# Performance work log

Measured on AMD Instinct MI355X. Metric: run time of the kernel, lower is better.

Reference implementation:

```python
import jax, jax.numpy as jnp
import numpy as np
from jax import lax

N, T, E = 20000, 64, 640000
H, OUT, HEADS = 128, 64, 3
NEG_SLOPE = 0.2  # GATConv default negative_slope


def setup_inputs() -> dict:
    key = jax.random.key(0)
    ks = jax.random.split(key, 10)
    s = 0.1
    return {
        "node_features": jax.random.normal(ks[0], (N, T), jnp.float32),
        "edge_index": jax.random.randint(ks[1], (2, E), 0, N, dtype=jnp.int32),
        "edge_attributes": jax.random.uniform(ks[2], (E,), jnp.float32),
        "lstm_Wih": jax.random.normal(ks[3], (4 * H, 1), jnp.float32) * s,
        "lstm_Whh": jax.random.normal(ks[4], (4 * H, H), jnp.float32) * s,
        "lstm_bih": jnp.zeros((4 * H,), jnp.float32),
        "lstm_bhh": jnp.zeros((4 * H,), jnp.float32),
        "gcn_W": jax.random.normal(ks[5], (H, H), jnp.float32) * s,
        "gcn_b": jnp.zeros((H,), jnp.float32),
        "gat_W": jax.random.normal(ks[6], (HEADS * OUT, H), jnp.float32) * s,
        "gat_att_src": jax.random.normal(ks[7], (HEADS, OUT), jnp.float32) * s,
        "gat_att_dst": jax.random.normal(ks[8], (HEADS, OUT), jnp.float32) * s,
        "gat_b": jnp.zeros((HEADS * OUT,), jnp.float32),
    }


def _lstm_last(x, Wih, Whh, bih, bhh):
    """x: [N, T, 1] -> last hidden state [N, H] (torch gate order i,f,g,o)."""
    n = x.shape[0]
    h_dim = Whh.shape[1]
    b = bih + bhh

    def step(carry, xt):
        h, c = carry
        g = xt @ Wih.T + h @ Whh.T + b  # [N, 4H]
        i, f, gg, o = jnp.split(g, 4, axis=-1)
        c = jax.nn.sigmoid(f) * c + jax.nn.sigmoid(i) * jnp.tanh(gg)
        h = jax.nn.sigmoid(o) * jnp.tanh(c)
        return (h, c), None

    init = (jnp.zeros((n, h_dim), x.dtype), jnp.zeros((n, h_dim), x.dtype))
    (h, _), _ = lax.scan(step, init, jnp.swapaxes(x, 0, 1))
    return h


def _add_self_loops(row, col, n):
    loop = jnp.arange(n, dtype=row.dtype)
    return jnp.concatenate([row, loop]), jnp.concatenate([col, loop])


def _gcn(x, row, col, edge_weight, W, b):
    """PyG GCNConv: self-loops (weight 1), symmetric normalization, W x + b."""
    n = x.shape[0]
    row, col = _add_self_loops(row, col, n)
    ew = jnp.concatenate([edge_weight, jnp.ones((n,), edge_weight.dtype)])
    x = x @ W.T  # [N, H]
    deg = jax.ops.segment_sum(ew, col, num_segments=n)
    dinv = jnp.where(deg > 0, deg ** -0.5, 0.0)
    norm = dinv[row] * ew * dinv[col]  # [E+N]
    out = jax.ops.segment_sum(x[row] * norm[:, None], col, num_segments=n)
    return out + b


def _gat(x, row, col, W, att_src, att_dst, b):
    """PyG GATConv (concat=True): self-loops, edge softmax over incoming edges."""
    n = x.shape[0]
    heads, c = att_src.shape
    xh = (x @ W.T).reshape(n, heads, c)  # [N, Hd, C]
    a_src = jnp.einsum('nhc,hc->nh', xh, att_src)  # [N, Hd]
    a_dst = jnp.einsum('nhc,hc->nh', xh, att_dst)
    row, col = _add_self_loops(row, col, n)
    alpha = jax.nn.leaky_relu(a_src[row] + a_dst[col], NEG_SLOPE)  # [E', Hd]
    amax = jax.ops.segment_max(alpha, col, num_segments=n)
    alpha = jnp.exp(alpha - amax[col])
    denom = jax.ops.segment_sum(alpha, col, num_segments=n)
    alpha = alpha / denom[col]
    out = jax.ops.segment_sum(xh[row] * alpha[:, :, None], col, num_segments=n)
    return out.reshape(n, heads * c) + b


def reference(node_features, edge_index, edge_attributes,
              lstm_Wih, lstm_Whh, lstm_bih, lstm_bhh,
              gcn_W, gcn_b, gat_W, gat_att_src, gat_att_dst, gat_b):
    x = node_features[:, :, None]  # [N, T, 1]
    x = _lstm_last(x, lstm_Wih, lstm_Whh, lstm_bih, lstm_bhh)  # [N, H]
    x = jax.nn.relu(x)
    row, col = edge_index[0], edge_index[1]
    x = _gcn(x, row, col, edge_attributes, gcn_W, gcn_b)
    x = jax.nn.relu(x)
    x = _gat(x, row, col, gat_W, gat_att_src, gat_att_dst, gat_b)  # [N, Hd*C]
    return jnp.mean(x, axis=0, keepdims=True)  # global_mean_pool, batch=None -> [1, Hd*C]
```

## Files before the change

### kernel.cpp

```cpp
#include <hip/hip_runtime.h>


#define N_NODES 20000
#define T_STEPS 64
#define N_EDGES 640000
#define HDIM    128
#define JOUT    192
#define NEG_SLOPE 0.2f
#define EDGE_CAP 128
#define NBW     16
#define NGRP    5
#define NBB     (NBW * NGRP)
#define BTHR    640
#define NBLK    250
#define GRIDX   256
#define LDS_W     131072
#define LDS_BW    4096
#define LDS_SCR   (NGRP * 4096)
#define LDS_FLG   256
#define LDS_TOTAL (LDS_W + LDS_BW + LDS_SCR + LDS_FLG)

#define L2E  1.4426950408889634f
#define K2E  2.8853900817779268f

typedef _Float16 half8 __attribute__((ext_vector_type(8)));
typedef _Float16 half4v __attribute__((ext_vector_type(4)));
typedef _Float16 half2v __attribute__((ext_vector_type(2)));
typedef float floatx4 __attribute__((ext_vector_type(4)));

__device__ __forceinline__ float lrelu(float x) { return x > 0.f ? x : NEG_SLOPE * x; }

__global__ __launch_bounds__(256) void prep_kernel(
    const float* __restrict__ Whh, _Float16* __restrict__ Wpack,
    const float* __restrict__ gcnW, _Float16* __restrict__ WpackG,
    const float* __restrict__ gatW, _Float16* __restrict__ WpackA,
    int* __restrict__ cnt, float* __restrict__ Wgt, float* __restrict__ accum)
{
  const int b = blockIdx.x;
  const int tid = threadIdx.x;
  if (b < 32) {
    int i = b * 256 + tid;
    int tile = i >> 6, lane = i & 63;
    int nt = tile >> 2, kt = tile & 3;
    int row = nt * 16 + (lane & 15);
    int c0  = kt * 32 + (lane >> 4) * 8;
    const float sc = ((row >> 7) == 2) ? K2E : L2E;
    half8 v;
    #pragma unroll
    for (int j = 0; j < 8; ++j)
      v[j] = (_Float16)(Whh[row * 128 + c0 + j] * sc);
    *(half8*)&Wpack[(size_t)i * 8] = v;
  } else if (b < 40) {
    int i = (b - 32) * 256 + tid;
    int tile = i >> 6, lane = i & 63;
    int mt = tile >> 2, kt = tile & 3;
    int row = mt * 16 + (lane & 15);
    int c0  = kt * 32 + (lane >> 4) * 8;
    half8 v;
    #pragma unroll
    for (int j = 0; j < 8; ++j) v[j] = (_Float16)gcnW[row * 128 + c0 + j];
    *(half8*)&WpackG[(size_t)i * 8] = v;
  } else if (b < 52) {
    int i = (b - 40) * 256 + tid;
    int tile = i >> 6, lane = i & 63;
    int mt = tile >> 2, kt = tile & 3;
    int row = mt * 16 + (lane & 15);
    int c0  = kt * 32 + (lane >> 4) * 8;
    half8 v;
    #pragma unroll
    for (int j = 0; j < 8; ++j) v[j] = (_Float16)gatW[row * 128 + c0 + j];
    *(half8*)&WpackA[(size_t)i * 8] = v;
  } else {
    int i = (b - 52) * 256 + tid;
    if (i < N_NODES) {
      cnt[i] = 0;
      *(float4*)&Wgt[i * 4] = make_float4(0.f, 0.f, 0.f, 0.f);
    }
    if (i < JOUT) accum[i] = 0.f;
  }
}


#define INITACC(L, acc) do {                                                  \
  _Pragma("unroll") for (int g_ = 0; g_ < 4; ++g_) {                          \
    const float4 p0_ = *(const float4*)&bwRole[g_ * 128 + (L) * 16];          \
    const float4 p1_ = *(const float4*)&bwRole[g_ * 128 + (L) * 16 + 2];      \
    acc[g_][0] = p0_.x + xv * p0_.y;                                          \
    acc[g_][1] = p0_.z + xv * p0_.w;                                          \
    acc[g_][2] = p1_.x + xv * p1_.y;                                          \
    acc[g_][3] = p1_.z + xv * p1_.w;                                          \
  }                                                                           \
} while (0)

#define LDA(buf, L, KT) do {                                                  \
  _Pragma("unroll") for (int g_ = 0; g_ < 4; ++g_)                            \
    buf[g_] = *(const half8*)&WlRole[g_ * 16384 + (L) * 2048 + (KT) * 512];   \
} while (0)

#define MFA(acc, buf, KT) do {                                                \
  _Pragma("unroll") for (int g_ = 0; g_ < 4; ++g_)                            \
    acc[g_] = __builtin_amdgcn_mfma_f32_16x16x32_f16(                         \
        buf[g_], Bf[(KT)], acc[g_], 0, 0, 0);                                 \
} while (0)

#define PHASE4(L, acc) do {                                                   \
  const int cg_ = cgb + (L);                                                  \
  half4v hpack;                                                               \
  _Pragma("unroll") for (int r_ = 0; r_ < 4; ++r_) {                          \
    const float Be = __builtin_amdgcn_exp2f(-acc[0][r_]);                     \
    const float Ae = __builtin_amdgcn_exp2f(-acc[1][r_]);                     \
    const float De = __builtin_amdgcn_exp2f(acc[2][r_]);                      \
    const float Ee = __builtin_amdgcn_exp2f(-acc[3][r_]);                     \
    const float Ap = Ae + 1.f;                                                \
    const float Bp = Be + 1.f;                                                \
    const float Dp = De + 1.f;                                                \
    const float Nn = cst[(L) * 4 + r_] * Bp * Dp + Ap * (De - 1.f);           \
    const float cv = Nn * __builtin_amdgcn_rcpf(Ap * Bp * Dp);                \
    cst[(L) * 4 + r_] = cv;                                                   \
    const float cvc = fminf(fmaxf(cv, -10.f), 10.f);                          \
    const float Fe = __builtin_amdgcn_exp2f(K2E * cvc);                       \
    hpack[r_] = (_Float16)((Fe - 1.f) *                                       \
                __builtin_amdgcn_rcpf((Ee + 1.f) * (Fe + 1.f)));              \
  }                                                                           \
  const int lp_ = nl + 16 * (2 * (cg_ & 1) + wq_hi);                          \
  *(half4v*)&myscr[(cg_ >> 1) * 512 + lp_ * 8 + j0] = hpack;                  \
} while (0)

#define SB __builtin_amdgcn_sched_barrier(0)

#define SIGNAL(arr, val) do {                                                 \
  __threadfence_block();                                                      \
  if (ln == 0) arr[wv] = (val);                                               \
} while (0)
#define WAITGE(arr, val) do {                                                 \
  if (ln == 0) { while (arr[pw] < (val)) __builtin_amdgcn_s_sleep(1); }       \
  __builtin_amdgcn_wave_barrier();                                            \
  __threadfence_block();                                                      \
} while (0)

#define LSTM_STEP(t) do {                                                     \
  WAITGE(flW, (t));                                                           \
  half8 Bf[4];                                                                \
  _Pragma("unroll") for (int kt_ = 0; kt_ < 4; ++kt_)                         \
    Bf[kt_] = *(const half8*)&scrLane[kt_ * 512];                             \
  SIGNAL(flR, (t) + 1);                                                       \
  floatx4 accA[4], accB[4];                                                   \
  half8 Aa[4], Ab[4];                                                         \
                                                                  \
  INITACC(0, accA);                                                           \
  LDA(Aa, 0, 0); LDA(Ab, 0, 1);                                               \
  MFA(accA, Aa, 0); LDA(Aa, 0, 2);                                            \
  MFA(accA, Ab, 1); LDA(Ab, 0, 3);                                            \
  MFA(accA, Aa, 2); MFA(accA, Ab, 3);                                         \
                                                                  \
  INITACC(1, accB); LDA(Aa, 1, 0); LDA(Ab, 1, 1);                             \
  WAITGE(flR, (t) + 1);                                                       \
  SB; PHASE4(0, accA);                                                        \
  MFA(accB, Aa, 0); LDA(Aa, 1, 2);                                            \
  MFA(accB, Ab, 1); LDA(Ab, 1, 3);                                            \
  MFA(accB, Aa, 2); MFA(accB, Ab, 3);                                         \
                                                                  \
  INITACC(2, accA); LDA(Aa, 2, 0); LDA(Ab, 2, 1);                             \
  SB; PHASE4(1, accB);                                                        \
  MFA(accA, Aa, 0); LDA(Aa, 2, 2);                                            \
  MFA(accA, Ab, 1); LDA(Ab, 2, 3);                                            \
  MFA(accA, Aa, 2); MFA(accA, Ab, 3);                                         \
                                                                  \
  INITACC(3, accB); LDA(Aa, 3, 0); LDA(Ab, 3, 1);                             \
  SB; PHASE4(2, accA);                                                        \
  MFA(accB, Aa, 0); LDA(Aa, 3, 2);                                            \
  MFA(accB, Ab, 1); LDA(Ab, 3, 3);                                            \
  MFA(accB, Aa, 2); MFA(accB, Ab, 3);                                         \
  PHASE4(3, accB);                                                            \
  SIGNAL(flW, (t) + 1);                                                       \
} while (0)

__global__ __attribute__((amdgpu_flat_work_group_size(BTHR, BTHR),
                          amdgpu_waves_per_eu(3, 3)))
void lstm_stream_kernel(
    const float* __restrict__ xfeat, const _Float16* __restrict__ Wpack,
    const float* __restrict__ Wih, const float* __restrict__ bih,
    const float* __restrict__ bhh, _Float16* __restrict__ x1,
    const int* __restrict__ ei, const float* __restrict__ ew,
    int* __restrict__ cnt, int2* __restrict__ pairB)
{
  const int tid  = threadIdx.x;

  if (blockIdx.x >= NBLK) {
    const int stride = (GRIDX - NBLK) * BTHR;
    for (int e = (blockIdx.x - NBLK) * BTHR + tid; e < N_EDGES; e += stride) {
      const int r = ei[e];
      const int c = ei[N_EDGES + e];
      const float w = ew[e];
      const int p = atomicAdd(&cnt[c], 1);
      pairB[(size_t)c * EDGE_CAP + p] = make_int2(r, __float_as_int(w));
    }
    return;
  }

  extern __shared__ char dynlds[];
  _Float16* Wl  = (_Float16*)dynlds;
  float2*   bw  = (float2*)(dynlds + LDS_W);
  _Float16* scr = (_Float16*)(dynlds + LDS_W + LDS_BW);
  volatile int* flR = (volatile int*)(dynlds + LDS_W + LDS_BW + LDS_SCR);
  volatile int* flW = flR + 16;

  const int wv   = tid >> 6;
  const int pw   = wv ^ 1;
  const int grp  = wv >> 1;
  const int role = wv & 1;
  const int cgb  = role * 4;
  const int ln   = tid & 63;
  const int nl   = ln & 15;
  const int quad = ln >> 4;
  const int n0   = blockIdx.x * NBB + grp * NBW;

  {
    const float4* src = (const float4*)Wpack;
    float4* dst = (float4*)Wl;
    for (int i = tid; i < LDS_W / 16; i += BTHR) dst[i] = src[i];
  }
  for (int i = tid; i < 512; i += BTHR) {
    const float sc = ((i >> 7) == 2) ? K2E : L2E;
    bw[i] = make_float2((bih[i] + bhh[i]) * sc, Wih[i] * sc);
  }
  {
    float4* z = (float4*)scr;
    for (int i = tid; i < LDS_SCR / 16; i += BTHR)
      z[i] = make_float4(0.f, 0.f, 0.f, 0.f);
  }
  if (tid < 32) { flR[tid] = 0; flW[tid] = 0; }
  __syncthreads();

  _Float16* myscr = scr + grp * 2048;
  const _Float16* WlRole  = Wl + (size_t)cgb * 2048 + (size_t)ln * 8;
  const float2*   bwRole  = bw + cgb * 16 + quad * 4;
  const _Float16* scrLane = myscr + (size_t)ln * 8;
  const float* xrow = xfeat + (size_t)(n0 + nl) * T_STEPS;

  float cst[16];
  #pragma unroll
  for (int i = 0; i < 16; ++i) cst[i] = 0.f;

  const int wq_hi = quad >> 1;
  const int j0    = (quad & 1) * 4;

  float xv = xrow[0];

  #pragma unroll 1
  for (int t = 0; t < T_STEPS; ++t) {
    const float xn = xrow[(t + 1 <= 63) ? (t + 1) : 63];
    LSTM_STEP(t);
    xv = xn;
  }

  #pragma unroll
  for (int k = 0; k < 2; ++k) {
    const int kt = role * 2 + k;
    half8 hf = *(const half8*)&scrLane[kt * 512];
    #pragma unroll
    for (int j = 0; j < 8; ++j)
      hf[j] = (_Float16)fmaxf((float)hf[j], 0.f);
    *(half8*)&x1[(size_t)(n0 + nl) * HDIM + kt * 32 + quad * 8] = hf;
  }
}

__global__ __launch_bounds__(256) void degdinv_kernel(
    const int* __restrict__ cnt, const int2* __restrict__ pairB,
    float* __restrict__ dinv)
{
  const int lane = threadIdx.x & 63;
  const int wv = threadIdx.x >> 6;
  const int c = blockIdx.x * 4 + wv;
  const int cc = cnt[c];
  const size_t base = (size_t)c * EDGE_CAP;
  float s = 0.f;
  for (int k = lane; k < cc; k += 64)
    s += __int_as_float(pairB[base + k].y);
  #pragma unroll
  for (int off = 1; off < 64; off <<= 1) s += __shfl_xor(s, off);
  if (lane == 0) dinv[c] = rsqrtf(s + 1.0f);
}

__global__ __launch_bounds__(256) void agg_gemm_att_kernel(
    const _Float16* __restrict__ x1, const float* __restrict__ dinv,
    const int* __restrict__ cnt, const int2* __restrict__ pairB,
    const float* __restrict__ gcn_b,
    const _Float16* __restrict__ PG, const _Float16* __restrict__ PA,
    const float* __restrict__ att_src, const float* __restrict__ att_dst,
    _Float16* __restrict__ xh, float4* __restrict__ asrc,
    float4* __restrict__ adst)
{
  __shared__ float2 stg[4][64];
  __shared__ _Float16 z[16][132];
  __shared__ _Float16 zz[16][132];
  __shared__ float aS[JOUT], aD[JOUT];
  __shared__ float sAp[4][16][3], sDp[4][16][3];

  const int tid = threadIdx.x;
  const int ln = tid & 63;
  const int wv = tid >> 6;
  const int quad = ln >> 4;
  const int nl = ln & 15;
  const int nb = blockIdx.x * 16;

  for (int i = tid; i < JOUT; i += 256) { aS[i] = att_src[i]; aD[i] = att_dst[i]; }

  const half2v* x12 = (const half2v*)x1;
  #pragma unroll 1
  for (int d = 0; d < 4; ++d) {
    const int c = nb + wv * 4 + d;
    const float dc = dinv[c];
    const half2v xc = x12[c * 64 + ln];
    float ax = (float)xc[0] * dc * dc, ay = (float)xc[1] * dc * dc;
    const int cc = cnt[c];
    const size_t base = (size_t)c * EDGE_CAP;
    for (int tb = 0; tb < cc; tb += 64) {
      const int ne = min(64, cc - tb);
      const int k = tb + ln;
      if (k < cc) {
        const int2 pr = pairB[base + k];
        stg[wv][ln] = make_float2(__int_as_float(pr.x),
                                  __int_as_float(pr.y) * dinv[pr.x] * dc);
      }
      __builtin_amdgcn_wave_barrier();
      int i = 0;
      for (; i + 4 <= ne; i += 4) {
        float2 p0 = stg[wv][i],     p1 = stg[wv][i + 1];
        float2 p2 = stg[wv][i + 2], p3 = stg[wv][i + 3];
        const half2v a0 = x12[(size_t)__float_as_int(p0.x) * 64 + ln];
        const half2v a1 = x12[(size_t)__float_as_int(p1.x) * 64 + ln];
        const half2v a2 = x12[(size_t)__float_as_int(p2.x) * 64 + ln];
        const half2v a3 = x12[(size_t)__float_as_int(p3.x) * 64 + ln];
        ax += (float)a0[0] * p0.y + (float)a1[0] * p1.y +
              (float)a2[0] * p2.y + (float)a3[0] * p3.y;
        ay += (float)a0[1] * p0.y + (float)a1[1] * p1.y +
              (float)a2[1] * p2.y + (float)a3[1] * p3.y;
      }
      for (; i < ne; ++i) {
        float2 p0 = stg[wv][i];
        const half2v a0 = x12[(size_t)__float_as_int(p0.x) * 64 + ln];
        ax += (float)a0[0] * p0.y; ay += (float)a0[1] * p0.y;
      }
      __builtin_amdgcn_wave_barrier();
    }
    const int dn = wv * 4 + d;
    half2v o; o[0] = (_Float16)ax; o[1] = (_Float16)ay;
    *(half2v*)&z[dn][ln * 2] = o;
  }
  __syncthreads();

  {
    half8 Bf[4];
    #pragma unroll
    for (int kt = 0; kt < 4; ++kt)
      Bf[kt] = *(const half8*)&z[nl][kt * 32 + quad * 8];
    #pragma unroll
    for (int mm = 0; mm < 2; ++mm) {
      const int m = wv * 2 + mm;
      floatx4 acc = {0.f, 0.f, 0.f, 0.f};
      #pragma unroll
      for (int kt = 0; kt < 4; ++kt) {
        const half8 Af = *(const half8*)&PG[(size_t)((m * 4 + kt) * 64 + ln) * 8];
        acc = __builtin_amdgcn_mfma_f32_16x16x32_f16(Af, Bf[kt], acc, 0, 0, 0);
      }
      #pragma unroll
      for (int j = 0; j < 4; ++j) {
        const int jj = m * 16 + quad * 4 + j;
        zz[nl][jj] = (_Float16)fmaxf(acc[j] + gcn_b[jj], 0.f);
      }
    }
  }
  __syncthreads();

  {
    half8 Bf[4];
    #pragma unroll
    for (int kt = 0; kt < 4; ++kt)
      Bf[kt] = *(const half8*)&zz[nl][kt * 32 + quad * 8];
    float sA[3] = {0.f, 0.f, 0.f}, sD[3] = {0.f, 0.f, 0.f};
    #pragma unroll
    for (int mm = 0; mm < 3; ++mm) {
      const int m = wv * 3 + mm;
      floatx4 acc = {0.f, 0.f, 0.f, 0.f};
      #pragma unroll
      for (int kt = 0; kt < 4; ++kt) {
        const half8 Af = *(const half8*)&PA[(size_t)((m * 4 + kt) * 64 + ln) * 8];
        acc = __builtin_amdgcn_mfma_f32_16x16x32_f16(Af, Bf[kt], acc, 0, 0, 0);
      }
      const int h  = m >> 2;
      const int jo = (m & 3) * 16 + quad * 4;
      half4v o;
      #pragma unroll
      for (int j = 0; j < 4; ++j) {
        sA[h] += acc[j] * aS[h * 64 + jo + j];
        sD[h] += acc[j] * aD[h * 64 + jo + j];
        o[j] = (_Float16)acc[j];
      }
      *(half4v*)&xh[(size_t)(nb + nl) * JOUT + m * 16 + quad * 4] = o;
    }
    #pragma unroll
    for (int h = 0; h < 3; ++h) {
      sA[h] += __shfl_xor(sA[h], 16); sA[h] += __shfl_xor(sA[h], 32);
      sD[h] += __shfl_xor(sD[h], 16); sD[h] += __shfl_xor(sD[h], 32);
    }
    if (quad == 0) {
      #pragma unroll
      for (int h = 0; h < 3; ++h) {
        sAp[wv][nl][h] = sA[h];
        sDp[wv][nl][h] = sD[h];
      }
    }
  }
  __syncthreads();
  if (tid < 16) {
    float a0 = 0.f, a1 = 0.f, a2 = 0.f, d0 = 0.f, d1 = 0.f, d2 = 0.f;
    #pragma unroll
    for (int w = 0; w < 4; ++w) {
      a0 += sAp[w][tid][0]; a1 += sAp[w][tid][1]; a2 += sAp[w][tid][2];
      d0 += sDp[w][tid][0]; d1 += sDp[w][tid][1]; d2 += sDp[w][tid][2];
    }
    asrc[nb + tid] = make_float4(a0, a1, a2, 0.f);
    adst[nb + tid] = make_float4(d0, d1, d2, 0.f);
  }
}

__global__ __launch_bounds__(256) void gat_weight_kernel(
    const float4* __restrict__ asrc, const float4* __restrict__ adst,
    const int* __restrict__ cnt, const int2* __restrict__ pairB,
    float* __restrict__ W)
{
  const int lane = threadIdx.x & 63;
  const int wv = threadIdx.x >> 6;
  const int c = blockIdx.x * 4 + wv;
  const int cc = cnt[c];
  const size_t base = (size_t)c * EDGE_CAP;
  const float4 adc = adst[c];
  const float4 asc = asrc[c];
  const float se0 = __expf(lrelu(asc.x + adc.x));
  const float se1 = __expf(lrelu(asc.y + adc.y));
  const float se2 = __expf(lrelu(asc.z + adc.z));
  float dp0 = 0.f, dp1 = 0.f, dp2 = 0.f;
  float a0v[2], a1v[2], a2v[2]; int sv[2];
  #pragma unroll
  for (int it = 0; it < 2; ++it) {
    const int k = it * 64 + lane;
    sv[it] = -1;
    a0v[it] = 0.f; a1v[it] = 0.f; a2v[it] = 0.f;
    if (k < cc) {
      const int s = pairB[base + k].x;
      const float4 av = asrc[s];
      const float a0 = __expf(lrelu(av.x + adc.x));
      const float a1 = __expf(lrelu(av.y + adc.y));
      const float a2 = __expf(lrelu(av.z + adc.z));
      dp0 += a0; dp1 += a1; dp2 += a2;
      sv[it] = s; a0v[it] = a0; a1v[it] = a1; a2v[it] = a2;
    }
  }
  #pragma unroll
  for (int off = 1; off < 64; off <<= 1) {
    dp0 += __shfl_xor(dp0, off);
    dp1 += __shfl_xor(dp1, off);
    dp2 += __shfl_xor(dp2, off);
  }
  const float iv0 = 1.f / (dp0 + se0);
  const float iv1 = 1.f / (dp1 + se1);
  const float iv2 = 1.f / (dp2 + se2);
  if (lane == 0) {
    atomicAdd(&W[c * 4 + 0], se0 * iv0);
    atomicAdd(&W[c * 4 + 1], se1 * iv1);
    atomicAdd(&W[c * 4 + 2], se2 * iv2);
  }
  #pragma unroll
  for (int it = 0; it < 2; ++it) {
    if (sv[it] >= 0) {
      atomicAdd(&W[sv[it] * 4 + 0], a0v[it] * iv0);
      atomicAdd(&W[sv[it] * 4 + 1], a1v[it] * iv1);
      atomicAdd(&W[sv[it] * 4 + 2], a2v[it] * iv2);
    }
  }
}

__global__ __launch_bounds__(192) void gat_final_kernel(
    const _Float16* __restrict__ xh, const float* __restrict__ W,
    float* __restrict__ accum)
{
  const int j = threadIdx.x;
  const int h = j >> 6;
  float sum = 0.f;
  const int s0 = blockIdx.x * 80;
  for (int s = s0; s < s0 + 80; ++s)
    sum += W[s * 4 + h] * (float)xh[(size_t)s * JOUT + j];
  atomicAdd(&accum[j], sum);
}

__global__ void finalize_kernel(const float* __restrict__ accum,
                                const float* __restrict__ gat_b,
                                float* __restrict__ out)
{
  int j = threadIdx.x;
  if (j < JOUT) out[j] = accum[j] * (1.0f / N_NODES) + gat_b[j];
}

extern "C" void kernel_launch(void* const* d_in, const int* in_sizes, int n_in,
                              void* d_out, int out_size, void* d_ws, size_t ws_size,
                              hipStream_t stream)
{
  const float* xfeat = (const float*)d_in[0];
  const int*   eidx  = (const int*)d_in[1];
  const float* eattr = (const float*)d_in[2];
  const float* Wih   = (const float*)d_in[3];
  const float* Whh   = (const float*)d_in[4];
  const float* bihp  = (const float*)d_in[5];
  const float* bhhp  = (const float*)d_in[6];
  const float* gcnW  = (const float*)d_in[7];
  const float* gcnb  = (const float*)d_in[8];
  const float* gatW  = (const float*)d_in[9];
  const float* attS  = (const float*)d_in[10];
  const float* attD  = (const float*)d_in[11];
  const float* gatb  = (const float*)d_in[12];
  float* out = (float*)d_out;

  char* ws = (char*)d_ws;
  size_t off = 0;
  auto alloc = [&](size_t bytes) {
    char* p = ws + off;
    off += (bytes + 255) & ~size_t(255);
    return p;
  };
  _Float16*  x1     = (_Float16*)alloc((size_t)N_NODES * 128 * 2);
  _Float16*  xh     = (_Float16*)alloc((size_t)N_NODES * 192 * 2);
  float4*    asrc   = (float4*)alloc((size_t)N_NODES * 16);
  float4*    adst   = (float4*)alloc((size_t)N_NODES * 16);
  float*     dinv   = (float*)alloc((size_t)N_NODES * 4);
  int*       cnt    = (int*)alloc((size_t)N_NODES * 4);
  int2*      pairB  = (int2*)alloc((size_t)N_NODES * EDGE_CAP * 8);
  float*     Wgt    = (float*)alloc((size_t)N_NODES * 4 * 4);
  float*     accum  = (float*)alloc(JOUT * 4);
  _Float16*  wpack  = (_Float16*)alloc(131072);
  _Float16*  wpackG = (_Float16*)alloc((size_t)128 * 128 * 2);
  _Float16*  wpackA = (_Float16*)alloc((size_t)192 * 128 * 2);

  hipFuncSetAttribute((const void*)lstm_stream_kernel,
                      hipFuncAttributeMaxDynamicSharedMemorySize, LDS_TOTAL);

  prep_kernel<<<131, 256, 0, stream>>>(Whh, wpack, gcnW, wpackG, gatW, wpackA,
                                       cnt, Wgt, accum);
  lstm_stream_kernel<<<GRIDX, BTHR, LDS_TOTAL, stream>>>(
      xfeat, wpack, Wih, bihp, bhhp, x1, eidx, eattr, cnt, pairB);
  degdinv_kernel<<<N_NODES / 4, 256, 0, stream>>>(cnt, pairB, dinv);
  agg_gemm_att_kernel<<<N_NODES / 16, 256, 0, stream>>>(
      x1, dinv, cnt, pairB, gcnb, wpackG, wpackA, attS, attD, xh, asrc, adst);
  gat_weight_kernel<<<N_NODES / 4, 256, 0, stream>>>(asrc, adst, cnt, pairB, Wgt);
  gat_final_kernel<<<N_NODES / 80, 192, 0, stream>>>(xh, Wgt, accum);
  finalize_kernel<<<1, 256, 0, stream>>>(accum, gatb, out);
}
```

Baseline: 554.9 us.

## Split LSTM handshake into half-ready flags and fold degree into edge bucketing

```diff
diff --git a/kernel.cpp b/kernel.cpp
--- a/kernel.cpp
+++ b/kernel.cpp
@@ -34,7 +34,8 @@
     const float* __restrict__ Whh, _Float16* __restrict__ Wpack,
     const float* __restrict__ gcnW, _Float16* __restrict__ WpackG,
     const float* __restrict__ gatW, _Float16* __restrict__ WpackA,
-    int* __restrict__ cnt, float* __restrict__ Wgt, float* __restrict__ accum)
+    int* __restrict__ cnt, float* __restrict__ deg,
+    float* __restrict__ Wgt, float* __restrict__ accum)
 {
   const int b = blockIdx.x;
   const int tid = threadIdx.x;
@@ -74,6 +75,7 @@
     int i = (b - 52) * 256 + tid;
     if (i < N_NODES) {
       cnt[i] = 0;
+      deg[i] = 0.f;
       *(float4*)&Wgt[i * 4] = make_float4(0.f, 0.f, 0.f, 0.f);
     }
     if (i < JOUT) accum[i] = 0.f;
@@ -138,20 +140,24 @@
   __threadfence_block();                                                      \
 } while (0)
 
-#define LSTM_STEP(t) do {                                                     \
-  WAITGE(flW, (t));                                                           \
+#define LSTM_STEP(t, K0, K1, K2, K3) do {                                     \
   half8 Bf[4];                                                                \
-  _Pragma("unroll") for (int kt_ = 0; kt_ < 4; ++kt_)                         \
-    Bf[kt_] = *(const half8*)&scrLane[kt_ * 512];                             \
-  SIGNAL(flR, (t) + 1);                                                       \
+  Bf[K0] = *(const half8*)&scrLane[(K0) * 512];                               \
+  Bf[K1] = *(const half8*)&scrLane[(K1) * 512];                               \
   floatx4 accA[4], accB[4];                                                   \
   half8 Aa[4], Ab[4];                                                         \
-                                                                  \
+              \
   INITACC(0, accA);                                                           \
-  LDA(Aa, 0, 0); LDA(Ab, 0, 1);                                               \
-  MFA(accA, Aa, 0); LDA(Aa, 0, 2);                                            \
-  MFA(accA, Ab, 1); LDA(Ab, 0, 3);                                            \
-  MFA(accA, Aa, 2); MFA(accA, Ab, 3);                                         \
+  LDA(Aa, 0, K0); LDA(Ab, 0, K1);                                             \
+  MFA(accA, Aa, K0); LDA(Aa, 0, K2);                                          \
+  MFA(accA, Ab, K1); LDA(Ab, 0, K3);                                          \
+  WAITGE(flWh, (t));                                                          \
+  Bf[K2] = *(const half8*)&scrLane[(K2) * 512];                               \
+  MFA(accA, Aa, K2);                                                          \
+  WAITGE(flW, (t));                                                           \
+  Bf[K3] = *(const half8*)&scrLane[(K3) * 512];                               \
+  MFA(accA, Ab, K3);                                                          \
+  SIGNAL(flR, (t) + 1);                                                       \
                                                                   \
   INITACC(1, accB); LDA(Aa, 1, 0); LDA(Ab, 1, 1);                             \
   WAITGE(flR, (t) + 1);                                                       \
@@ -162,6 +168,7 @@
                                                                   \
   INITACC(2, accA); LDA(Aa, 2, 0); LDA(Ab, 2, 1);                             \
   SB; PHASE4(1, accB);                                                        \
+  SIGNAL(flWh, (t) + 1);                         \
   MFA(accA, Aa, 0); LDA(Aa, 2, 2);                                            \
   MFA(accA, Ab, 1); LDA(Ab, 2, 3);                                            \
   MFA(accA, Aa, 2); MFA(accA, Ab, 3);                                         \
@@ -182,7 +189,7 @@
     const float* __restrict__ Wih, const float* __restrict__ bih,
     const float* __restrict__ bhh, _Float16* __restrict__ x1,
     const int* __restrict__ ei, const float* __restrict__ ew,
-    int* __restrict__ cnt, int2* __restrict__ pairB)
+    int* __restrict__ cnt, int2* __restrict__ pairB, float* __restrict__ deg)
 {
   const int tid  = threadIdx.x;
 
@@ -194,6 +201,7 @@
       const float w = ew[e];
       const int p = atomicAdd(&cnt[c], 1);
       pairB[(size_t)c * EDGE_CAP + p] = make_int2(r, __float_as_int(w));
+      atomicAdd(&deg[c], w);
     }
     return;
   }
@@ -202,8 +210,9 @@
   _Float16* Wl  = (_Float16*)dynlds;
   float2*   bw  = (float2*)(dynlds + LDS_W);
   _Float16* scr = (_Float16*)(dynlds + LDS_W + LDS_BW);
-  volatile int* flR = (volatile int*)(dynlds + LDS_W + LDS_BW + LDS_SCR);
-  volatile int* flW = flR + 16;
+  volatile int* flR  = (volatile int*)(dynlds + LDS_W + LDS_BW + LDS_SCR);
+  volatile int* flW  = flR + 16;
+  volatile int* flWh = flR + 32;
 
   const int wv   = tid >> 6;
   const int pw   = wv ^ 1;
@@ -229,7 +238,7 @@
     for (int i = tid; i < LDS_SCR / 16; i += BTHR)
       z[i] = make_float4(0.f, 0.f, 0.f, 0.f);
   }
-  if (tid < 32) { flR[tid] = 0; flW[tid] = 0; }
+  if (tid < 48) { flR[tid] = 0; }
   __syncthreads();
 
   _Float16* myscr = scr + grp * 2048;
@@ -247,11 +256,20 @@
 
   float xv = xrow[0];
 
-  #pragma unroll 1
-  for (int t = 0; t < T_STEPS; ++t) {
-    const float xn = xrow[(t + 1 <= 63) ? (t + 1) : 63];
-    LSTM_STEP(t);
-    xv = xn;
+  if (role == 0) {
+    #pragma unroll 1
+    for (int t = 0; t < T_STEPS; ++t) {
+      const float xn = xrow[(t + 1 <= 63) ? (t + 1) : 63];
+      LSTM_STEP(t, 0, 1, 2, 3);
+      xv = xn;
+    }
+  } else {
+    #pragma unroll 1
+    for (int t = 0; t < T_STEPS; ++t) {
+      const float xn = xrow[(t + 1 <= 63) ? (t + 1) : 63];
+      LSTM_STEP(t, 2, 3, 0, 1);
+      xv = xn;
+    }
   }
 
   #pragma unroll
@@ -265,25 +283,8 @@
   }
 }
 
-__global__ __launch_bounds__(256) void degdinv_kernel(
-    const int* __restrict__ cnt, const int2* __restrict__ pairB,
-    float* __restrict__ dinv)
-{
-  const int lane = threadIdx.x & 63;
-  const int wv = threadIdx.x >> 6;
-  const int c = blockIdx.x * 4 + wv;
-  const int cc = cnt[c];
-  const size_t base = (size_t)c * EDGE_CAP;
-  float s = 0.f;
-  for (int k = lane; k < cc; k += 64)
-    s += __int_as_float(pairB[base + k].y);
-  #pragma unroll
-  for (int off = 1; off < 64; off <<= 1) s += __shfl_xor(s, off);
-  if (lane == 0) dinv[c] = rsqrtf(s + 1.0f);
-}
-
 __global__ __launch_bounds__(256) void agg_gemm_att_kernel(
-    const _Float16* __restrict__ x1, const float* __restrict__ dinv,
+    const _Float16* __restrict__ x1, const float* __restrict__ deg,
     const int* __restrict__ cnt, const int2* __restrict__ pairB,
     const float* __restrict__ gcn_b,
     const _Float16* __restrict__ PG, const _Float16* __restrict__ PA,
@@ -310,7 +311,7 @@
   #pragma unroll 1
   for (int d = 0; d < 4; ++d) {
     const int c = nb + wv * 4 + d;
-    const float dc = dinv[c];
+    const float dc = rsqrtf(deg[c] + 1.0f);
     const half2v xc = x12[c * 64 + ln];
     float ax = (float)xc[0] * dc * dc, ay = (float)xc[1] * dc * dc;
     const int cc = cnt[c];
@@ -321,7 +322,7 @@
       if (k < cc) {
         const int2 pr = pairB[base + k];
         stg[wv][ln] = make_float2(__int_as_float(pr.x),
-                                  __int_as_float(pr.y) * dinv[pr.x] * dc);
+            __int_as_float(pr.y) * rsqrtf(deg[pr.x] + 1.0f) * dc);
       }
       __builtin_amdgcn_wave_barrier();
       int i = 0;
@@ -532,7 +533,7 @@
   _Float16*  xh     = (_Float16*)alloc((size_t)N_NODES * 192 * 2);
   float4*    asrc   = (float4*)alloc((size_t)N_NODES * 16);
   float4*    adst   = (float4*)alloc((size_t)N_NODES * 16);
-  float*     dinv   = (float*)alloc((size_t)N_NODES * 4);
+  float*     deg    = (float*)alloc((size_t)N_NODES * 4);
   int*       cnt    = (int*)alloc((size_t)N_NODES * 4);
   int2*      pairB  = (int2*)alloc((size_t)N_NODES * EDGE_CAP * 8);
   float*     Wgt    = (float*)alloc((size_t)N_NODES * 4 * 4);
@@ -545,12 +546,11 @@
                       hipFuncAttributeMaxDynamicSharedMemorySize, LDS_TOTAL);
 
   prep_kernel<<<131, 256, 0, stream>>>(Whh, wpack, gcnW, wpackG, gatW, wpackA,
-                                       cnt, Wgt, accum);
+                                       cnt, deg, Wgt, accum);
   lstm_stream_kernel<<<GRIDX, BTHR, LDS_TOTAL, stream>>>(
-      xfeat, wpack, Wih, bihp, bhhp, x1, eidx, eattr, cnt, pairB);
-  degdinv_kernel<<<N_NODES / 4, 256, 0, stream>>>(cnt, pairB, dinv);
+      xfeat, wpack, Wih, bihp, bhhp, x1, eidx, eattr, cnt, pairB, deg);
   agg_gemm_att_kernel<<<N_NODES / 16, 256, 0, stream>>>(
-      x1, dinv, cnt, pairB, gcnb, wpackG, wpackA, attS, attD, xh, asrc, adst);
+      x1, deg, cnt, pairB, gcnb, wpackG, wpackA, attS, attD, xh, asrc, adst);
   gat_weight_kernel<<<N_NODES / 4, 256, 0, stream>>>(asrc, adst, cnt, pairB, Wgt);
   gat_final_kernel<<<N_NODES / 80, 192, 0, stream>>>(xh, Wgt, accum);
   finalize_kernel<<<1, 256, 0, stream>>>(accum, gatb, out);
```

New measurement: 728.3 us. 31.2% more time.
